# Performance work log

Measured on AMD Instinct MI355X. Metric: run time of the kernel, lower is better.

## Reference

```python
import jax, jax.numpy as jnp
import numpy as np
from jax import lax

GAMMA = 5.0
BETA = -2.5
EPS_EDGE = 1e-6
EPS_STD = 1e-6


def _fixed_kernels():
    """Stack 3 Sobel-x, 3 Sobel-y and Laplacian kernels, zero-padded to 7x7.
    Zero-padding a kernel symmetrically + padding=3 conv is mathematically
    identical to the per-scale padding=scale//2 convs in the original.
    Channel order: gx3, gy3, gx5, gy5, gx7, gy7, lap."""
    s3 = np.array([[-1, 0, 1], [-2, 0, 2], [-1, 0, 1]], np.float32)
    s5 = np.array([[-1, -2, 0, 2, 1], [-4, -8, 0, 8, 4], [-6, -12, 0, 12, 6],
                   [-4, -8, 0, 8, 4], [-1, -2, 0, 2, 1]], np.float32)
    s7 = np.array([[-1, -4, -5, 0, 5, 4, 1], [-6, -24, -30, 0, 30, 24, 6],
                   [-15, -60, -75, 0, 75, 60, 15], [-20, -80, -100, 0, 100, 80, 20],
                   [-15, -60, -75, 0, 75, 60, 15], [-6, -24, -30, 0, 30, 24, 6],
                   [-1, -4, -5, 0, 5, 4, 1]], np.float32)
    lap = np.array([[0, 1, 0], [1, -4, 1], [0, 1, 0]], np.float32)
    ks = []
    for k in (s3, s3.T, s5, s5.T, s7, s7.T, lap):
        p = (7 - k.shape[0]) // 2
        ks.append(np.pad(k, p))
    return jnp.asarray(np.stack(ks)[:, None])  # [7,1,7,7] OIHW


_KERNELS = _fixed_kernels()


def setup_inputs() -> dict:
    key = jax.random.key(0)
    x = jax.random.normal(key, (16, 64, 256, 256), dtype=jnp.float32)
    return {"x": x}


def reference(x):
    # grayscale: mean over channels -> [B,1,H,W]
    x_gray = x.mean(axis=1, keepdims=True)
    # single grouped conv producing all 7 filtered maps: [B,7,H,W]
    g = lax.conv_general_dilated(
        x_gray, _KERNELS.astype(x.dtype), window_strides=(1, 1),
        padding=((3, 3), (3, 3)),
        dimension_numbers=("NCHW", "OIHW", "NCHW"))
    gx = g[:, 0:6:2]  # [B,3,H,W]
    gy = g[:, 1:6:2]  # [B,3,H,W]
    edges = jnp.sqrt(gx * gx + gy * gy + EPS_EDGE)      # [B,3,H,W]
    lap_edge = jnp.abs(g[:, 6:7])                        # [B,1,H,W]
    # mean over the 4 concatenated edge channels
    combined = (edges.sum(axis=1, keepdims=True) + lap_edge) / 4.0  # [B,1,H,W]
    # per-image normalization (torch .std is unbiased -> ddof=1)
    mu = combined.mean(axis=(2, 3), keepdims=True)
    sigma = jnp.std(combined, axis=(2, 3), keepdims=True, ddof=1) + EPS_STD
    normalized = (combined - mu) / sigma
    boundary_map = jax.nn.sigmoid(GAMMA * normalized + BETA)
    return x * (1.0 + boundary_map)
```

## Files before the change

kernel.cpp:

```cpp
#include <hip/hip_runtime.h>
#include <math.h>

#define N_IMG 16
#define CCH   64
#define H     256
#define W     256
#define HW    (H*W)
#define HW4   (HW/4)
#define TS    16

typedef float fx4 __attribute__((ext_vector_type(4)));

__global__ __launch_bounds__(256) void gray_kernel(const float4* __restrict__ x,
                                                   float4* __restrict__ gray) {
    int bid = blockIdx.x;
    int n   = bid >> 6;
    int p4  = ((bid & 63) << 8) + threadIdx.x;
    const float4* xp = x + (size_t)n * CCH * HW4 + p4;
    float4 acc = make_float4(0.f, 0.f, 0.f, 0.f);
    #pragma unroll 8
    for (int c = 0; c < CCH; ++c) {
        float4 v = xp[(size_t)c * HW4];
        acc.x += v.x; acc.y += v.y; acc.z += v.z; acc.w += v.w;
    }
    const float s = 1.0f / 64.0f;
    acc.x *= s; acc.y *= s; acc.z *= s; acc.w *= s;
    gray[(size_t)n * HW4 + p4] = acc;
}

__global__ __launch_bounds__(256) void conv_kernel(const float* __restrict__ gray,
                                                   float* __restrict__ comb,
                                                   float2* __restrict__ part) {
    __shared__ float t[TS + 6][TS + 7];
    __shared__ float rs[256];
    __shared__ float rq[256];
    int n  = blockIdx.z;
    int h0 = blockIdx.y * TS - 3;
    int w0 = blockIdx.x * TS - 3;
    const float* g = gray + (size_t)n * HW;

    int tid = threadIdx.y * TS + threadIdx.x;
    for (int i = tid; i < 22 * 22; i += 256) {
        int r  = i / 22, c2 = i - r * 22;
        int hh = h0 + r, ww = w0 + c2;
        t[r][c2] = (hh >= 0 && hh < H && ww >= 0 && ww < W) ? g[hh * W + ww] : 0.f;
    }
    __syncthreads();

    int ty = threadIdx.y, tx = threadIdx.x;
    float v[7][7];
    #pragma unroll
    for (int i = 0; i < 7; ++i)
        #pragma unroll
        for (int j = 0; j < 7; ++j)
            v[i][j] = t[ty + i][tx + j];

    float gx7 = 0.f, gy7 = 0.f;
    {
        const float vw[7] = {1.f, 6.f, 15.f, 20.f, 15.f, 6.f, 1.f};
        const float dw[7] = {-1.f, -4.f, -5.f, 0.f, 5.f, 4.f, 1.f};
        #pragma unroll
        for (int i = 0; i < 7; ++i) {
            float rh = -v[i][0] - 4.f*v[i][1] - 5.f*v[i][2] + 5.f*v[i][4] + 4.f*v[i][5] + v[i][6];
            float rsu =  v[i][0] + 6.f*v[i][1] + 15.f*v[i][2] + 20.f*v[i][3] + 15.f*v[i][4] + 6.f*v[i][5] + v[i][6];
            gx7 += vw[i] * rh;
            gy7 += dw[i] * rsu;
        }
    }
    float gx5 = 0.f, gy5 = 0.f;
    {
        const float vw[5] = {1.f, 4.f, 6.f, 4.f, 1.f};
        const float dw[5] = {-1.f, -2.f, 0.f, 2.f, 1.f};
        #pragma unroll
        for (int i = 0; i < 5; ++i) {
            float rh = -v[i+1][1] - 2.f*v[i+1][2] + 2.f*v[i+1][4] + v[i+1][5];
            float rsu =  v[i+1][1] + 4.f*v[i+1][2] + 6.f*v[i+1][3] + 4.f*v[i+1][4] + v[i+1][5];
            gx5 += vw[i] * rh;
            gy5 += dw[i] * rsu;
        }
    }
    float gx3 = 0.f, gy3 = 0.f;
    {
        const float vw[3] = {1.f, 2.f, 1.f};
        const float dw[3] = {-1.f, 0.f, 1.f};
        #pragma unroll
        for (int i = 0; i < 3; ++i) {
            float rh = v[i+2][4] - v[i+2][2];
            float rsu = v[i+2][2] + 2.f*v[i+2][3] + v[i+2][4];
            gx3 += vw[i] * rh;
            gy3 += dw[i] * rsu;
        }
    }
    float lap = v[2][3] + v[4][3] + v[3][2] + v[3][4] - 4.f*v[3][3];

    float e3 = sqrtf(gx3*gx3 + gy3*gy3 + 1e-6f);
    float e5 = sqrtf(gx5*gx5 + gy5*gy5 + 1e-6f);
    float e7 = sqrtf(gx7*gx7 + gy7*gy7 + 1e-6f);
    float combined = (e3 + e5 + e7 + fabsf(lap)) * 0.25f;

    comb[(size_t)n * HW + (size_t)(h0 + 3 + ty) * W + (w0 + 3 + tx)] = combined;

    rs[tid] = combined;
    rq[tid] = combined * combined;
    __syncthreads();
    for (int off = 128; off > 0; off >>= 1) {
        if (tid < off) {
            rs[tid] += rs[tid + off];
            rq[tid] += rq[tid + off];
        }
        __syncthreads();
    }
    if (tid == 0) {
        int blockLin = blockIdx.y * (W / TS) + blockIdx.x;
        part[n * 256 + blockLin] = make_float2(rs[0], rq[0]);
    }
}

__global__ __launch_bounds__(256) void stats_kernel(const float2* __restrict__ part,
                                                    float2* __restrict__ stats) {
    __shared__ float ssum[256];
    __shared__ float ssq[256];
    int n = blockIdx.x;
    float2 p = part[n * 256 + threadIdx.x];
    ssum[threadIdx.x] = p.x;
    ssq[threadIdx.x]  = p.y;
    __syncthreads();
    for (int off = 128; off > 0; off >>= 1) {
        if ((int)threadIdx.x < off) {
            ssum[threadIdx.x] += ssum[threadIdx.x + off];
            ssq[threadIdx.x]  += ssq[threadIdx.x + off];
        }
        __syncthreads();
    }
    if (threadIdx.x == 0) {
        float mu  = ssum[0] / (float)HW;
        float var = (ssq[0] - (float)HW * mu * mu) / (float)(HW - 1);
        var = fmaxf(var, 0.f);
        float sigma = sqrtf(var) + 1e-6f;
        stats[n] = make_float2(mu, 1.0f / sigma);
    }
}

__global__ __launch_bounds__(256) void mul_kernel(const float4* __restrict__ x,
                                                  const float4* __restrict__ comb4,
                                                  const float2* __restrict__ stats,
                                                  fx4* __restrict__ out) {
    const size_t total = (size_t)N_IMG * CCH * HW4;
    size_t stride = (size_t)gridDim.x * 256;
    for (size_t i = (size_t)blockIdx.x * 256 + threadIdx.x; i < total; i += stride) {
        int p4 = (int)(i & (HW4 - 1));
        int n  = (int)(i >> 20);
        float2 st = stats[n];
        float4 c = comb4[((size_t)n << 14) + p4];
        float4 v = x[i];
        fx4 r;
        r.x = v.x * (1.0f + 1.0f / (1.0f + __expf(2.5f - 5.0f * (c.x - st.x) * st.y)));
        r.y = v.y * (1.0f + 1.0f / (1.0f + __expf(2.5f - 5.0f * (c.y - st.x) * st.y)));
        r.z = v.z * (1.0f + 1.0f / (1.0f + __expf(2.5f - 5.0f * (c.z - st.x) * st.y)));
        r.w = v.w * (1.0f + 1.0f / (1.0f + __expf(2.5f - 5.0f * (c.w - st.x) * st.y)));
        __builtin_nontemporal_store(r, &out[i]);
    }
}

extern "C" void kernel_launch(void* const* d_in, const int* in_sizes, int n_in,
                              void* d_out, int out_size, void* d_ws, size_t ws_size,
                              hipStream_t stream) {
    const float* x = (const float*)d_in[0];
    float* out = (float*)d_out;
    char* ws = (char*)d_ws;

    float*  gray  = (float*)ws;
    float*  comb  = (float*)(ws + (size_t)N_IMG * HW * 4);
    float2* part  = (float2*)(ws + (size_t)2 * N_IMG * HW * 4);
    float2* stats = (float2*)(ws + (size_t)2 * N_IMG * HW * 4 + 4096 * sizeof(float2));

    gray_kernel<<<N_IMG * 64, 256, 0, stream>>>((const float4*)x, (float4*)gray);

    dim3 cgrid(W / TS, H / TS, N_IMG);
    conv_kernel<<<cgrid, dim3(TS, TS), 0, stream>>>(gray, comb, part);

    stats_kernel<<<N_IMG, 256, 0, stream>>>(part, stats);

    mul_kernel<<<2048, 256, 0, stream>>>((const float4*)x, (const float4*)comb,
                                         stats, (fx4*)out);
}
```

Baseline: 165.4 us.

## Fuse gray, conv, stats and multiply into one cooperative persistent kernel

Replaces the four kernel launches with a single cooperative kernel of 1024 blocks that uses grid.sync() between the grayscale, convolution, statistics and modulation phases. Each block now handles four conv tiles and produces one partial sum, and the stats phase reduces 64 partials per image. The intent is to remove launch overhead and inter-kernel gaps. In exchange it adds grid-wide barriers and fixes the grid size for the memory-bound phases, which may reduce memory-level parallelism compared with the separate launches.

```diff
diff --git a/kernel.cpp b/kernel.cpp
--- a/kernel.cpp
+++ b/kernel.cpp
@@ -1,5 +1,8 @@
 #include <hip/hip_runtime.h>
+#include <hip/hip_cooperative_groups.h>
 #include <math.h>
+
+namespace cg = cooperative_groups;
 
 #define N_IMG 16
 #define CCH   64
@@ -8,179 +11,192 @@
 #define HW    (H*W)
 #define HW4   (HW/4)
 #define TS    16
+#define NBLK  1024
+#define NTHR  256
 
 typedef float fx4 __attribute__((ext_vector_type(4)));
 
-__global__ __launch_bounds__(256) void gray_kernel(const float4* __restrict__ x,
-                                                   float4* __restrict__ gray) {
-    int bid = blockIdx.x;
-    int n   = bid >> 6;
-    int p4  = ((bid & 63) << 8) + threadIdx.x;
-    const float4* xp = x + (size_t)n * CCH * HW4 + p4;
-    float4 acc = make_float4(0.f, 0.f, 0.f, 0.f);
-    #pragma unroll 8
-    for (int c = 0; c < CCH; ++c) {
-        float4 v = xp[(size_t)c * HW4];
-        acc.x += v.x; acc.y += v.y; acc.z += v.z; acc.w += v.w;
-    }
-    const float s = 1.0f / 64.0f;
-    acc.x *= s; acc.y *= s; acc.z *= s; acc.w *= s;
-    gray[(size_t)n * HW4 + p4] = acc;
-}
-
-__global__ __launch_bounds__(256) void conv_kernel(const float* __restrict__ gray,
-                                                   float* __restrict__ comb,
-                                                   float2* __restrict__ part) {
+__global__ __launch_bounds__(NTHR, 4) void fused_kernel(
+    const float4* __restrict__ x,
+    float4* __restrict__ gray4,
+    float*  __restrict__ comb,
+    float2* __restrict__ part,
+    float2* __restrict__ stats,
+    fx4*    __restrict__ out)
+{
+    cg::grid_group grid = cg::this_grid();
+
     __shared__ float t[TS + 6][TS + 7];
     __shared__ float rs[256];
     __shared__ float rq[256];
-    int n  = blockIdx.z;
-    int h0 = blockIdx.y * TS - 3;
-    int w0 = blockIdx.x * TS - 3;
-    const float* g = gray + (size_t)n * HW;
-
-    int tid = threadIdx.y * TS + threadIdx.x;
-    for (int i = tid; i < 22 * 22; i += 256) {
-        int r  = i / 22, c2 = i - r * 22;
-        int hh = h0 + r, ww = w0 + c2;
-        t[r][c2] = (hh >= 0 && hh < H && ww >= 0 && ww < W) ? g[hh * W + ww] : 0.f;
-    }
-    __syncthreads();
-
-    int ty = threadIdx.y, tx = threadIdx.x;
-    float v[7][7];
-    #pragma unroll
-    for (int i = 0; i < 7; ++i)
-        #pragma unroll
-        for (int j = 0; j < 7; ++j)
-            v[i][j] = t[ty + i][tx + j];
-
-    float gx7 = 0.f, gy7 = 0.f;
+
+    const int tid = threadIdx.x;
+    const int b   = blockIdx.x;
+    const int g   = b * NTHR + tid;
+
     {
-        const float vw[7] = {1.f, 6.f, 15.f, 20.f, 15.f, 6.f, 1.f};
-        const float dw[7] = {-1.f, -4.f, -5.f, 0.f, 5.f, 4.f, 1.f};
-        #pragma unroll
-        for (int i = 0; i < 7; ++i) {
-            float rh = -v[i][0] - 4.f*v[i][1] - 5.f*v[i][2] + 5.f*v[i][4] + 4.f*v[i][5] + v[i][6];
-            float rsu =  v[i][0] + 6.f*v[i][1] + 15.f*v[i][2] + 20.f*v[i][3] + 15.f*v[i][4] + 6.f*v[i][5] + v[i][6];
-            gx7 += vw[i] * rh;
-            gy7 += dw[i] * rsu;
-        }
-    }
-    float gx5 = 0.f, gy5 = 0.f;
+        int n  = g >> 14;
+        int p4 = g & (HW4 - 1);
+        const float4* xp = x + (size_t)n * CCH * HW4 + p4;
+        float4 acc = make_float4(0.f, 0.f, 0.f, 0.f);
+        #pragma unroll 8
+        for (int c = 0; c < CCH; ++c) {
+            float4 v = xp[(size_t)c * HW4];
+            acc.x += v.x; acc.y += v.y; acc.z += v.z; acc.w += v.w;
+        }
+        const float s = 1.0f / 64.0f;
+        acc.x *= s; acc.y *= s; acc.z *= s; acc.w *= s;
+        gray4[(size_t)n * HW4 + p4] = acc;
+    }
+    grid.sync();
+
     {
-        const float vw[5] = {1.f, 4.f, 6.f, 4.f, 1.f};
-        const float dw[5] = {-1.f, -2.f, 0.f, 2.f, 1.f};
-        #pragma unroll
-        for (int i = 0; i < 5; ++i) {
-            float rh = -v[i+1][1] - 2.f*v[i+1][2] + 2.f*v[i+1][4] + v[i+1][5];
-            float rsu =  v[i+1][1] + 4.f*v[i+1][2] + 6.f*v[i+1][3] + 4.f*v[i+1][4] + v[i+1][5];
-            gx5 += vw[i] * rh;
-            gy5 += dw[i] * rsu;
-        }
-    }
-    float gx3 = 0.f, gy3 = 0.f;
+        const float* gray = (const float*)gray4;
+        float psum = 0.f, psq = 0.f;
+        #pragma unroll 1
+        for (int j = 0; j < 4; ++j) {
+            int t_idx = b * 4 + j;
+            int n     = t_idx >> 8;
+            int wim   = t_idx & 255;
+            int h0    = (wim >> 4) * TS - 3;
+            int w0    = (wim & 15) * TS - 3;
+            const float* gptr = gray + (size_t)n * HW;
+
+            for (int i = tid; i < 22 * 22; i += 256) {
+                int r  = i / 22, c2 = i - r * 22;
+                int hh = h0 + r, ww = w0 + c2;
+                t[r][c2] = (hh >= 0 && hh < H && ww >= 0 && ww < W) ? gptr[hh * W + ww] : 0.f;
+            }
+            __syncthreads();
+
+            int ty = tid >> 4, tx = tid & 15;
+            float v[7][7];
+            #pragma unroll
+            for (int i = 0; i < 7; ++i)
+                #pragma unroll
+                for (int jj = 0; jj < 7; ++jj)
+                    v[i][jj] = t[ty + i][tx + jj];
+
+            float gx7 = 0.f, gy7 = 0.f;
+            {
+                const float vw[7] = {1.f, 6.f, 15.f, 20.f, 15.f, 6.f, 1.f};
+                const float dw[7] = {-1.f, -4.f, -5.f, 0.f, 5.f, 4.f, 1.f};
+                #pragma unroll
+                for (int i = 0; i < 7; ++i) {
+                    float rh  = -v[i][0] - 4.f*v[i][1] - 5.f*v[i][2] + 5.f*v[i][4] + 4.f*v[i][5] + v[i][6];
+                    float rsu =  v[i][0] + 6.f*v[i][1] + 15.f*v[i][2] + 20.f*v[i][3] + 15.f*v[i][4] + 6.f*v[i][5] + v[i][6];
+                    gx7 += vw[i] * rh;
+                    gy7 += dw[i] * rsu;
+                }
+            }
+            float gx5 = 0.f, gy5 = 0.f;
+            {
+                const float vw[5] = {1.f, 4.f, 6.f, 4.f, 1.f};
+                const float dw[5] = {-1.f, -2.f, 0.f, 2.f, 1.f};
+                #pragma unroll
+                for (int i = 0; i < 5; ++i) {
+                    float rh  = -v[i+1][1] - 2.f*v[i+1][2] + 2.f*v[i+1][4] + v[i+1][5];
+                    float rsu =  v[i+1][1] + 4.f*v[i+1][2] + 6.f*v[i+1][3] + 4.f*v[i+1][4] + v[i+1][5];
+                    gx5 += vw[i] * rh;
+                    gy5 += dw[i] * rsu;
+                }
+            }
+            float gx3 = 0.f, gy3 = 0.f;
+            {
+                const float vw[3] = {1.f, 2.f, 1.f};
+                const float dw[3] = {-1.f, 0.f, 1.f};
+                #pragma unroll
+                for (int i = 0; i < 3; ++i) {
+                    float rh  = v[i+2][4] - v[i+2][2];
+                    float rsu = v[i+2][2] + 2.f*v[i+2][3] + v[i+2][4];
+                    gx3 += vw[i] * rh;
+                    gy3 += dw[i] * rsu;
+                }
+            }
+            float lap = v[2][3] + v[4][3] + v[3][2] + v[3][4] - 4.f*v[3][3];
+
+            float e3 = sqrtf(gx3*gx3 + gy3*gy3 + 1e-6f);
+            float e5 = sqrtf(gx5*gx5 + gy5*gy5 + 1e-6f);
+            float e7 = sqrtf(gx7*gx7 + gy7*gy7 + 1e-6f);
+            float combined = (e3 + e5 + e7 + fabsf(lap)) * 0.25f;
+
+            comb[(size_t)n * HW + (size_t)(h0 + 3 + ty) * W + (w0 + 3 + tx)] = combined;
+            psum += combined;
+            psq  += combined * combined;
+            __syncthreads();
+        }
+
+        rs[tid] = psum;
+        rq[tid] = psq;
+        __syncthreads();
+        for (int off = 128; off > 0; off >>= 1) {
+            if (tid < off) {
+                rs[tid] += rs[tid + off];
+                rq[tid] += rq[tid + off];
+            }
+            __syncthreads();
+        }
+        if (tid == 0) part[b] = make_float2(rs[0], rq[0]);
+    }
+    grid.sync();
+
+    if (b < N_IMG) {
+        if (tid < 64) {
+            float2 p = part[b * 64 + tid];
+            rs[tid] = p.x;
+            rq[tid] = p.y;
+        }
+        __syncthreads();
+        for (int off = 32; off > 0; off >>= 1) {
+            if (tid < off) {
+                rs[tid] += rs[tid + off];
+                rq[tid] += rq[tid + off];
+            }
+            __syncthreads();
+        }
+        if (tid == 0) {
+            float mu  = rs[0] / (float)HW;
+            float var = (rq[0] - (float)HW * mu * mu) / (float)(HW - 1);
+            var = fmaxf(var, 0.f);
+            stats[b] = make_float2(mu, 1.0f / (sqrtf(var) + 1e-6f));
+        }
+    }
+    grid.sync();
+
     {
-        const float vw[3] = {1.f, 2.f, 1.f};
-        const float dw[3] = {-1.f, 0.f, 1.f};
-        #pragma unroll
-        for (int i = 0; i < 3; ++i) {
-            float rh = v[i+2][4] - v[i+2][2];
-            float rsu = v[i+2][2] + 2.f*v[i+2][3] + v[i+2][4];
-            gx3 += vw[i] * rh;
-            gy3 += dw[i] * rsu;
-        }
-    }
-    float lap = v[2][3] + v[4][3] + v[3][2] + v[3][4] - 4.f*v[3][3];
-
-    float e3 = sqrtf(gx3*gx3 + gy3*gy3 + 1e-6f);
-    float e5 = sqrtf(gx5*gx5 + gy5*gy5 + 1e-6f);
-    float e7 = sqrtf(gx7*gx7 + gy7*gy7 + 1e-6f);
-    float combined = (e3 + e5 + e7 + fabsf(lap)) * 0.25f;
-
-    comb[(size_t)n * HW + (size_t)(h0 + 3 + ty) * W + (w0 + 3 + tx)] = combined;
-
-    rs[tid] = combined;
-    rq[tid] = combined * combined;
-    __syncthreads();
-    for (int off = 128; off > 0; off >>= 1) {
-        if (tid < off) {
-            rs[tid] += rs[tid + off];
-            rq[tid] += rq[tid + off];
-        }
-        __syncthreads();
-    }
-    if (tid == 0) {
-        int blockLin = blockIdx.y * (W / TS) + blockIdx.x;
-        part[n * 256 + blockLin] = make_float2(rs[0], rq[0]);
-    }
-}
-
-__global__ __launch_bounds__(256) void stats_kernel(const float2* __restrict__ part,
-                                                    float2* __restrict__ stats) {
-    __shared__ float ssum[256];
-    __shared__ float ssq[256];
-    int n = blockIdx.x;
-    float2 p = part[n * 256 + threadIdx.x];
-    ssum[threadIdx.x] = p.x;
-    ssq[threadIdx.x]  = p.y;
-    __syncthreads();
-    for (int off = 128; off > 0; off >>= 1) {
-        if ((int)threadIdx.x < off) {
-            ssum[threadIdx.x] += ssum[threadIdx.x + off];
-            ssq[threadIdx.x]  += ssq[threadIdx.x + off];
-        }
-        __syncthreads();
-    }
-    if (threadIdx.x == 0) {
-        float mu  = ssum[0] / (float)HW;
-        float var = (ssq[0] - (float)HW * mu * mu) / (float)(HW - 1);
-        var = fmaxf(var, 0.f);
-        float sigma = sqrtf(var) + 1e-6f;
-        stats[n] = make_float2(mu, 1.0f / sigma);
-    }
-}
-
-__global__ __launch_bounds__(256) void mul_kernel(const float4* __restrict__ x,
-                                                  const float4* __restrict__ comb4,
-                                                  const float2* __restrict__ stats,
-                                                  fx4* __restrict__ out) {
-    const size_t total = (size_t)N_IMG * CCH * HW4;
-    size_t stride = (size_t)gridDim.x * 256;
-    for (size_t i = (size_t)blockIdx.x * 256 + threadIdx.x; i < total; i += stride) {
-        int p4 = (int)(i & (HW4 - 1));
-        int n  = (int)(i >> 20);
-        float2 st = stats[n];
-        float4 c = comb4[((size_t)n << 14) + p4];
-        float4 v = x[i];
-        fx4 r;
-        r.x = v.x * (1.0f + 1.0f / (1.0f + __expf(2.5f - 5.0f * (c.x - st.x) * st.y)));
-        r.y = v.y * (1.0f + 1.0f / (1.0f + __expf(2.5f - 5.0f * (c.y - st.x) * st.y)));
-        r.z = v.z * (1.0f + 1.0f / (1.0f + __expf(2.5f - 5.0f * (c.z - st.x) * st.y)));
-        r.w = v.w * (1.0f + 1.0f / (1.0f + __expf(2.5f - 5.0f * (c.w - st.x) * st.y)));
-        __builtin_nontemporal_store(r, &out[i]);
+        const float4* comb4 = (const float4*)comb;
+        const size_t total  = (size_t)N_IMG * CCH * HW4;
+        const size_t stride = (size_t)NBLK * NTHR;
+        for (size_t i = g; i < total; i += stride) {
+            int p4 = (int)(i & (HW4 - 1));
+            int n  = (int)(i >> 20);
+            float2 st = stats[n];
+            float4 c  = comb4[((size_t)n << 14) + p4];
+            float4 v  = x[i];
+            fx4 r;
+            r.x = v.x * (1.0f + 1.0f / (1.0f + __expf(2.5f - 5.0f * (c.x - st.x) * st.y)));
+            r.y = v.y * (1.0f + 1.0f / (1.0f + __expf(2.5f - 5.0f * (c.y - st.x) * st.y)));
+            r.z = v.z * (1.0f + 1.0f / (1.0f + __expf(2.5f - 5.0f * (c.z - st.x) * st.y)));
+            r.w = v.w * (1.0f + 1.0f / (1.0f + __expf(2.5f - 5.0f * (c.w - st.x) * st.y)));
+            __builtin_nontemporal_store(r, &out[i]);
+        }
     }
 }
 
 extern "C" void kernel_launch(void* const* d_in, const int* in_sizes, int n_in,
                               void* d_out, int out_size, void* d_ws, size_t ws_size,
                               hipStream_t stream) {
-    const float* x = (const float*)d_in[0];
-    float* out = (float*)d_out;
-    char* ws = (char*)d_ws;
-
-    float*  gray  = (float*)ws;
+    const float4* x   = (const float4*)d_in[0];
+    fx4*          out = (fx4*)d_out;
+    char*         ws  = (char*)d_ws;
+
+    float4* gray4 = (float4*)ws;
     float*  comb  = (float*)(ws + (size_t)N_IMG * HW * 4);
     float2* part  = (float2*)(ws + (size_t)2 * N_IMG * HW * 4);
-    float2* stats = (float2*)(ws + (size_t)2 * N_IMG * HW * 4 + 4096 * sizeof(float2));
-
-    gray_kernel<<<N_IMG * 64, 256, 0, stream>>>((const float4*)x, (float4*)gray);
-
-    dim3 cgrid(W / TS, H / TS, N_IMG);
-    conv_kernel<<<cgrid, dim3(TS, TS), 0, stream>>>(gray, comb, part);
-
-    stats_kernel<<<N_IMG, 256, 0, stream>>>(part, stats);
-
-    mul_kernel<<<2048, 256, 0, stream>>>((const float4*)x, (const float4*)comb,
-                                         stats, (fx4*)out);
+    float2* stats = (float2*)(ws + (size_t)2 * N_IMG * HW * 4 + NBLK * sizeof(float2));
+
+    void* args[] = { (void*)&x, (void*)&gray4, (void*)&comb,
+                     (void*)&part, (void*)&stats, (void*)&out };
+    hipLaunchCooperativeKernel((void*)fused_kernel, dim3(NBLK), dim3(NTHR),
+                               args, 0, stream);
 }
```

After: 488.8 us. 2.95x slower.
